# Performance work log

Measured on AMD Instinct MI355X. Metric: run time of the kernel, lower is better.

The kernel has to match this reference:

```python
import jax, jax.numpy as jnp
import numpy as np

B, IN, H = 4096, 1024, 1024


def setup_inputs() -> dict:
    key = jax.random.key(0)
    ks = jax.random.split(key, 6)
    s_h = 1.0 / np.sqrt(H)
    s_x = 1.0 / np.sqrt(IN)
    return {
        "x": jax.random.normal(ks[0], (B, IN), jnp.float32),
        "h": jax.random.normal(ks[1], (B, H), jnp.float32),
        "c": jax.random.normal(ks[2], (B, H), jnp.float32),
        # hidden_lin: Linear(H, 4H) with bias
        "Wh": jax.random.uniform(ks[3], (4 * H, H), jnp.float32, -s_h, s_h),
        "bh": jax.random.uniform(ks[4], (4 * H,), jnp.float32, -s_h, s_h),
        # input_lin: Linear(IN, 4H), bias=False
        "Wx": jax.random.uniform(ks[5], (4 * H, IN), jnp.float32, -s_x, s_x),
    }


def reference(x, h, c, Wh, bh, Wx):
    # ifgo = h @ Wh^T + bh + x @ Wx^T   -> [B, 4H]
    ifgo = jnp.dot(h, Wh.T) + bh + jnp.dot(x, Wx.T)
    i, f, g, o = jnp.split(ifgo, 4, axis=1)
    i = jax.nn.sigmoid(i)
    f = jax.nn.sigmoid(f)
    g = jnp.tanh(g)
    o = jax.nn.sigmoid(o)
    c_next = f * c + i * g
    h_next = o * jnp.tanh(c_next)
    return (h_next, c_next)
```

## Files before the change

### kernel.cpp

```cpp
#include <hip/hip_runtime.h>
#include <cstdint>
#include <cstddef>


#define NB   4096
#define KH   1024
#define KK   2048
#define ARR_ELEMS 4194304

typedef __bf16 bf16x8 __attribute__((ext_vector_type(8)));
typedef float  f32x4  __attribute__((ext_vector_type(4)));

__device__ inline unsigned short f2bf(float f) {
    union { float f; unsigned int u; } v; v.f = f;
    unsigned int u = v.u;
    u += 0x7FFFu + ((u >> 16) & 1u);
    return (unsigned short)(u >> 16);
}

__device__ inline float fsig(float v)  { return __builtin_amdgcn_rcpf(1.f + __expf(-v)); }
__device__ inline float ftanh(float v) { return 1.f - 2.f * __builtin_amdgcn_rcpf(1.f + __expf(2.f * v)); }

__global__ void convert_kernel(const float* __restrict__ h, const float* __restrict__ x,
                               const float* __restrict__ Wh, const float* __restrict__ Wx,
                               unsigned short* __restrict__ A, unsigned short* __restrict__ W) {
    int idx = blockIdx.x * 256 + threadIdx.x;
    int arr = idx >> 20;
    int off = (idx & 0xFFFFF) << 2;
    const float* src = (arr == 0) ? h : (arr == 1) ? x : (arr == 2) ? Wh : Wx;
    float4 v = *(const float4*)(src + off);
    unsigned int lo = (unsigned int)f2bf(v.x) | ((unsigned int)f2bf(v.y) << 16);
    unsigned int hi = (unsigned int)f2bf(v.z) | ((unsigned int)f2bf(v.w) << 16);
    uint2 packed; packed.x = lo; packed.y = hi;

    int row = off >> 10;
    int col = off & 1023;
    unsigned short* dst;
    size_t dstOff;
    if (arr < 2) {
        dst = A;
        dstOff = (size_t)row * KK + (arr == 1 ? 1024 : 0) + col;
    } else {
        int g = row >> 10, j = row & 1023;
        int p = ((j >> 4) << 6) | (g << 4) | (j & 15);
        dst = W;
        dstOff = (size_t)p * KK + (arr == 3 ? 1024 : 0) + col;
    }
    *(uint2*)(dst + dstOff) = packed;
}

__global__ void gemm_kernel(const unsigned short* __restrict__ A,
                            const unsigned short* __restrict__ W,
                            const float* __restrict__ bh,
                            const float* __restrict__ c,
                            float* __restrict__ out) {
    __shared__ __align__(16) unsigned short As[2 * 128 * 32];
    __shared__ __align__(16) unsigned short Bs[2 * 128 * 32];

    const int tid  = threadIdx.x;
    const int wave = tid >> 6;
    const int lane = tid & 63;
    const int tileN = blockIdx.x;
    const int tileM = blockIdx.y;

    const int stRow  = wave * 16 + (lane >> 2);
    const int stColE = (lane & 3) * 8;
    const unsigned short* gaBase = A + (size_t)(tileM * 128 + stRow) * KK + stColE;
    const unsigned short* gbBase = W + (size_t)(tileN * 128 + stRow) * KK + stColE;

    const int mBase = (wave >> 1) * 64;
    const int nBase = (wave & 1) * 64;
    const int fr = lane & 15;
    const int fk = (lane >> 4) * 8;

    f32x4 acc[4][4] = {};

    for (int kt = 0; kt < 32; ++kt) {
        const unsigned short* ga = gaBase + kt * 64;
        const unsigned short* gb = gbBase + kt * 64;
        #pragma unroll
        for (int i = 0; i < 4; ++i) {
            const int gOff = (i & 1) * 64 * KK + (i >> 1) * 32;
            const int lOff = i * 2048 + wave * 512;
            __builtin_amdgcn_global_load_lds(
                (const __attribute__((address_space(1))) void*)(ga + gOff),
                (__attribute__((address_space(3))) void*)(As + lOff), 16, 0, 0);
            __builtin_amdgcn_global_load_lds(
                (const __attribute__((address_space(1))) void*)(gb + gOff),
                (__attribute__((address_space(3))) void*)(Bs + lOff), 16, 0, 0);
        }

        __syncthreads();

        #pragma unroll
        for (int s = 0; s < 2; ++s) {
            bf16x8 a[4], b[4];
            #pragma unroll
            for (int i = 0; i < 4; ++i)
                a[i] = *(const bf16x8*)(As + s * 4096 + (mBase + i * 16 + fr) * 32 + fk);
            #pragma unroll
            for (int j = 0; j < 4; ++j)
                b[j] = *(const bf16x8*)(Bs + s * 4096 + (nBase + j * 16 + fr) * 32 + fk);

            #pragma unroll
            for (int i = 0; i < 4; ++i)
                #pragma unroll
                for (int j = 0; j < 4; ++j)
                    acc[i][j] = __builtin_amdgcn_mfma_f32_16x16x32_bf16(a[i], b[j], acc[i][j], 0, 0, 0);
        }

        __syncthreads();
    }

    const int j = ((tileN * 2 + (wave & 1)) << 4) | (lane & 15);
    const float bi = bh[j];
    const float bf = bh[j + 1024];
    const float bg = bh[j + 2048];
    const float bo = bh[j + 3072];

    const int row0 = tileM * 128 + mBase + (lane >> 4) * 4;

    float cv[4][4];
    #pragma unroll
    for (int i = 0; i < 4; ++i)
        #pragma unroll
        for (int r = 0; r < 4; ++r)
            cv[i][r] = c[(size_t)(row0 + i * 16 + r) * KH + j];

    #pragma unroll
    for (int i = 0; i < 4; ++i) {
        #pragma unroll
        for (int r = 0; r < 4; ++r) {
            const size_t idx = (size_t)(row0 + i * 16 + r) * KH + j;
            float iv = fsig(acc[i][0][r] + bi);
            float fv = fsig(acc[i][1][r] + bf);
            float gv = ftanh(acc[i][2][r] + bg);
            float ov = fsig(acc[i][3][r] + bo);
            float cn = fv * cv[i][r] + iv * gv;
            float hn = ov * ftanh(cn);
            out[idx] = hn;
            out[(size_t)ARR_ELEMS + idx] = cn;
        }
    }
}

extern "C" void kernel_launch(void* const* d_in, const int* in_sizes, int n_in,
                              void* d_out, int out_size, void* d_ws, size_t ws_size,
                              hipStream_t stream) {
    const float* x  = (const float*)d_in[0];
    const float* h  = (const float*)d_in[1];
    const float* c  = (const float*)d_in[2];
    const float* Wh = (const float*)d_in[3];
    const float* bh = (const float*)d_in[4];
    const float* Wx = (const float*)d_in[5];
    float* out = (float*)d_out;

    unsigned short* ws   = (unsigned short*)d_ws;
    unsigned short* Acat = ws;
    unsigned short* Wcat = ws + 2 * (size_t)ARR_ELEMS;

    convert_kernel<<<16384, 256, 0, stream>>>(h, x, Wh, Wx, Acat, Wcat);
    dim3 grid(32, 32);
    gemm_kernel<<<grid, 256, 0, stream>>>(Acat, Wcat, bh, c, out);
}
```

Baseline: 202.6 us.

## Rewrite GEMM as 256x256 tiles with double-buffered swizzled LDS pipeline

Grows the block tile from 128x128 to 256x256 with 8 waves, and double-buffers LDS with global_load_lds prefetch two k-tiles ahead. LDS reads use an XOR swizzle, interleaved with MFMA phases under s_setprio and explicit barriers and waitcnts. A remapped 1D grid is meant to improve L2 reuse. The goal is to raise MFMA utilization and hide global load latency. In exchange the kernel needs much more LDS and registers, runs only 256 blocks, and depends on fragile manual synchronization.

```diff
diff --git a/kernel.cpp b/kernel.cpp
--- a/kernel.cpp
+++ b/kernel.cpp
@@ -7,6 +7,7 @@
 #define KH   1024
 #define KK   2048
 #define ARR_ELEMS 4194304
+#define NKT  32
 
 typedef __bf16 bf16x8 __attribute__((ext_vector_type(8)));
 typedef float  f32x4  __attribute__((ext_vector_type(4)));
@@ -49,91 +50,168 @@
     *(uint2*)(dst + dstOff) = packed;
 }
 
-__global__ void gemm_kernel(const unsigned short* __restrict__ A,
+__global__ __launch_bounds__(512, 2) void gemm_kernel(const unsigned short* __restrict__ A,
                             const unsigned short* __restrict__ W,
                             const float* __restrict__ bh,
                             const float* __restrict__ c,
                             float* __restrict__ out) {
-    __shared__ __align__(16) unsigned short As[2 * 128 * 32];
-    __shared__ __align__(16) unsigned short Bs[2 * 128 * 32];
+    __shared__ __align__(16) unsigned short As[2 * 16384];
+    __shared__ __align__(16) unsigned short Bs[2 * 16384];
 
     const int tid  = threadIdx.x;
     const int wave = tid >> 6;
     const int lane = tid & 63;
-    const int tileN = blockIdx.x;
-    const int tileM = blockIdx.y;
-
-    const int stRow  = wave * 16 + (lane >> 2);
-    const int stColE = (lane & 3) * 8;
-    const unsigned short* gaBase = A + (size_t)(tileM * 128 + stRow) * KK + stColE;
-    const unsigned short* gbBase = W + (size_t)(tileN * 128 + stRow) * KK + stColE;
-
-    const int mBase = (wave >> 1) * 64;
-    const int nBase = (wave & 1) * 64;
-    const int fr = lane & 15;
-    const int fk = (lane >> 4) * 8;
-
-    f32x4 acc[4][4] = {};
-
-    for (int kt = 0; kt < 32; ++kt) {
-        const unsigned short* ga = gaBase + kt * 64;
-        const unsigned short* gb = gbBase + kt * 64;
-        #pragma unroll
-        for (int i = 0; i < 4; ++i) {
-            const int gOff = (i & 1) * 64 * KK + (i >> 1) * 32;
-            const int lOff = i * 2048 + wave * 512;
-            __builtin_amdgcn_global_load_lds(
-                (const __attribute__((address_space(1))) void*)(ga + gOff),
-                (__attribute__((address_space(3))) void*)(As + lOff), 16, 0, 0);
-            __builtin_amdgcn_global_load_lds(
-                (const __attribute__((address_space(1))) void*)(gb + gOff),
-                (__attribute__((address_space(3))) void*)(Bs + lOff), 16, 0, 0);
-        }
-
-        __syncthreads();
-
-        #pragma unroll
-        for (int s = 0; s < 2; ++s) {
-            bf16x8 a[4], b[4];
-            #pragma unroll
-            for (int i = 0; i < 4; ++i)
-                a[i] = *(const bf16x8*)(As + s * 4096 + (mBase + i * 16 + fr) * 32 + fk);
-            #pragma unroll
-            for (int j = 0; j < 4; ++j)
-                b[j] = *(const bf16x8*)(Bs + s * 4096 + (nBase + j * 16 + fr) * 32 + fk);
-
-            #pragma unroll
-            for (int i = 0; i < 4; ++i)
-                #pragma unroll
-                for (int j = 0; j < 4; ++j)
-                    acc[i][j] = __builtin_amdgcn_mfma_f32_16x16x32_bf16(a[i], b[j], acc[i][j], 0, 0, 0);
-        }
-
-        __syncthreads();
-    }
-
-    const int j = ((tileN * 2 + (wave & 1)) << 4) | (lane & 15);
-    const float bi = bh[j];
-    const float bf = bh[j + 1024];
-    const float bg = bh[j + 2048];
-    const float bo = bh[j + 3072];
-
-    const int row0 = tileM * 128 + mBase + (lane >> 4) * 4;
-
-    float cv[4][4];
-    #pragma unroll
-    for (int i = 0; i < 4; ++i)
+
+    const int bid   = (int)blockIdx.x;
+    const int swz   = (bid & 7) * 32 + (bid >> 3);
+    const int tileM = swz >> 4;
+    const int tileN = swz & 15;
+
+    const int wr  = wave >> 2;
+    const int wc  = wave & 3;
+    const int fr  = lane & 15;
+    const int fk2 = (lane >> 4) << 4;
+
+    const unsigned short* pa[4];
+    const unsigned short* pb[4];
+    #pragma unroll
+    for (int i = 0; i < 4; ++i) {
+        const int P   = (i * 512 + tid) * 16;
+        const int L   = P ^ (((P >> 7) & 7) << 4);
+        const int row = L >> 7;
+        const int kk  = (L & 127) >> 1;
+        pa[i] = A + (size_t)(tileM * 256 + row) * KK + kk;
+        pb[i] = W + (size_t)(tileN * 256 + row) * KK + kk;
+    }
+
+    const int swzm = (fr & 7) << 4;
+    int offA[8], offB[4];
+    #pragma unroll
+    for (int i = 0; i < 8; ++i)
+        offA[i] = (wr * 128 + i * 16 + fr) * 128 + (fk2 ^ swzm);
+    #pragma unroll
+    for (int j = 0; j < 4; ++j)
+        offB[j] = (wc * 64 + j * 16 + fr) * 128 + (fk2 ^ swzm);
+
+    f32x4 acc[8][4] = {};
+    bf16x8 afr[4][2], bfr[4][2];
+
+#define STAGE(KT, BUF) do { \
+    const size_t _ko = (size_t)(KT) * 64; \
+    _Pragma("unroll") \
+    for (int _i = 0; _i < 4; ++_i) { \
+        __builtin_amdgcn_global_load_lds( \
+            (const __attribute__((address_space(1))) void*)(pa[_i] + _ko), \
+            (__attribute__((address_space(3))) void*)(As + (BUF) * 16384 + _i * 4096 + wave * 512), 16, 0, 0); \
+        __builtin_amdgcn_global_load_lds( \
+            (const __attribute__((address_space(1))) void*)(pb[_i] + _ko), \
+            (__attribute__((address_space(3))) void*)(Bs + (BUF) * 16384 + _i * 4096 + wave * 512), 16, 0, 0); \
+    } \
+} while (0)
+
+#define MFMA16(IB, JB) do { \
+    _Pragma("unroll") \
+    for (int _i = 0; _i < 4; ++_i) \
+        _Pragma("unroll") \
+        for (int _j = 0; _j < 2; ++_j) \
+            _Pragma("unroll") \
+            for (int _s = 0; _s < 2; ++_s) \
+                acc[(IB) + _i][(JB) + _j] = __builtin_amdgcn_mfma_f32_16x16x32_bf16( \
+                    afr[_i][_s], bfr[(JB) + _j][_s], acc[(IB) + _i][(JB) + _j], 0, 0, 0); \
+} while (0)
+
+    STAGE(0, 0);
+    STAGE(1, 1);
+    asm volatile("s_waitcnt vmcnt(8)" ::: "memory");
+    asm volatile("s_barrier" ::: "memory");
+
+#define TILE(T, BUF) do { \
+    const char* AsB = (const char*)As + (BUF) * 32768; \
+    const char* BsB = (const char*)Bs + (BUF) * 32768; \
+     \
+    _Pragma("unroll") \
+    for (int i = 0; i < 4; ++i) { \
+        afr[i][0] = *(const bf16x8*)(AsB + offA[i]); \
+        afr[i][1] = *(const bf16x8*)(AsB + (offA[i] ^ 64)); \
+    } \
+    _Pragma("unroll") \
+    for (int j = 0; j < 2; ++j) { \
+        bfr[j][0] = *(const bf16x8*)(BsB + offB[j]); \
+        bfr[j][1] = *(const bf16x8*)(BsB + (offB[j] ^ 64)); \
+    } \
+    asm volatile("s_barrier" ::: "memory"); \
+    asm volatile("s_waitcnt lgkmcnt(0)" ::: "memory"); \
+    __builtin_amdgcn_s_setprio(1); \
+    MFMA16(0, 0); \
+    __builtin_amdgcn_s_setprio(0); \
+    asm volatile("s_barrier" ::: "memory"); \
+     \
+    _Pragma("unroll") \
+    for (int j = 2; j < 4; ++j) { \
+        bfr[j][0] = *(const bf16x8*)(BsB + offB[j]); \
+        bfr[j][1] = *(const bf16x8*)(BsB + (offB[j] ^ 64)); \
+    } \
+    asm volatile("s_barrier" ::: "memory"); \
+    asm volatile("s_waitcnt lgkmcnt(0)" ::: "memory"); \
+    __builtin_amdgcn_s_setprio(1); \
+    MFMA16(0, 2); \
+    __builtin_amdgcn_s_setprio(0); \
+    asm volatile("s_barrier" ::: "memory"); \
+     \
+    _Pragma("unroll") \
+    for (int i = 0; i < 4; ++i) { \
+        afr[i][0] = *(const bf16x8*)(AsB + offA[4 + i]); \
+        afr[i][1] = *(const bf16x8*)(AsB + (offA[4 + i] ^ 64)); \
+    } \
+    asm volatile("s_barrier" ::: "memory"); \
+    asm volatile("s_waitcnt lgkmcnt(0)" ::: "memory"); \
+    __builtin_amdgcn_s_setprio(1); \
+    MFMA16(4, 0); \
+    __builtin_amdgcn_s_setprio(0); \
+    asm volatile("s_barrier" ::: "memory"); \
+     \
+    { \
+        const int _ktc = ((T) + 2 <= NKT - 1) ? ((T) + 2) : (NKT - 1); \
+        STAGE(_ktc, BUF);  \
+    } \
+    asm volatile("s_barrier" ::: "memory"); \
+    __builtin_amdgcn_s_setprio(1); \
+    MFMA16(4, 2); \
+    __builtin_amdgcn_s_setprio(0); \
+    asm volatile("s_waitcnt vmcnt(8)" ::: "memory"); \
+    asm volatile("s_barrier" ::: "memory"); \
+} while (0)
+
+    for (int tt = 0; tt < NKT; tt += 2) {
+        TILE(tt, 0);
+        TILE(tt + 1, 1);
+    }
+#undef TILE
+#undef MFMA16
+#undef STAGE
+
+    const int j = ((tileN * 4 + wc) << 4) | fr;
+    const float bi  = bh[j];
+    const float bff = bh[j + 1024];
+    const float bg  = bh[j + 2048];
+    const float bo  = bh[j + 3072];
+
+    const int row0 = tileM * 256 + wr * 128 + (lane >> 4) * 4;
+
+    float cv[8][4];
+    #pragma unroll
+    for (int i = 0; i < 8; ++i)
         #pragma unroll
         for (int r = 0; r < 4; ++r)
             cv[i][r] = c[(size_t)(row0 + i * 16 + r) * KH + j];
 
     #pragma unroll
-    for (int i = 0; i < 4; ++i) {
+    for (int i = 0; i < 8; ++i) {
         #pragma unroll
         for (int r = 0; r < 4; ++r) {
             const size_t idx = (size_t)(row0 + i * 16 + r) * KH + j;
             float iv = fsig(acc[i][0][r] + bi);
-            float fv = fsig(acc[i][1][r] + bf);
+            float fv = fsig(acc[i][1][r] + bff);
             float gv = ftanh(acc[i][2][r] + bg);
             float ov = fsig(acc[i][3][r] + bo);
             float cn = fv * cv[i][r] + iv * gv;
@@ -160,6 +238,5 @@
     unsigned short* Wcat = ws + 2 * (size_t)ARR_ELEMS;
 
     convert_kernel<<<16384, 256, 0, stream>>>(h, x, Wh, Wx, Acat, Wcat);
-    dim3 grid(32, 32);
-    gemm_kernel<<<grid, 256, 0, stream>>>(Acat, Wcat, bh, c, out);
-}
+    gemm_kernel<<<256, 512, 0, stream>>>(Acat, Wcat, bh, c, out);
+}
```

Result: faster. 196.4 us (-3.1%).
